# Optimization experiments

Hardware: AMD Instinct MI355X
Metric: run time of the kernel (lower is better)

The kernel has to match this reference:

```python
import jax, jax.numpy as jnp
import numpy as np

WH, WW = 16, 16
NUM_HEADS = 16
DIM = 1024
BATCH = 64
SEQ = WH * WW + 1  # 257, includes cls token
NUM_REL = (2 * WH - 1) * (2 * WW - 1) + 3  # 964


def _make_rel_pos_index(wh, ww):
    # BEiT relative position index construction (intended semantics of the torch code)
    coords = np.stack(np.meshgrid(np.arange(wh), np.arange(ww), indexing='ij'))  # [2, wh, ww]
    flat = coords.reshape(2, -1)  # [2, wh*ww]
    rel = flat[:, :, None] - flat[:, None, :]  # [2, N-1, N-1]
    rel = rel.transpose(1, 2, 0).astype(np.int64)
    rel[:, :, 0] += wh - 1
    rel[:, :, 1] += ww - 1
    rel[:, :, 0] *= 2 * ww - 1
    num_rel = (2 * wh - 1) * (2 * ww - 1) + 3
    idx = np.zeros((wh * ww + 1, wh * ww + 1), dtype=np.int32)
    idx[1:, 1:] = rel.sum(-1)
    idx[0, :] = num_rel - 3  # cls-to-token
    idx[:, 0] = num_rel - 2  # token-to-cls
    idx[0, 0] = num_rel - 1  # cls-to-cls
    return idx


def setup_inputs() -> dict:
    key = jax.random.key(0)
    ks = jax.random.split(key, 7)
    return {
        'x': jax.random.normal(ks[0], (BATCH, SEQ, DIM), dtype=jnp.float32),
        'qkv_weight': jax.random.normal(ks[1], (3 * DIM, DIM), dtype=jnp.float32) * 0.02,
        'query_bias': jax.random.normal(ks[2], (DIM,), dtype=jnp.float32) * 0.02,
        'value_bias': jax.random.normal(ks[3], (DIM,), dtype=jnp.float32) * 0.02,
        'rel_pos_bias_table': jax.random.normal(ks[4], (NUM_REL, NUM_HEADS), dtype=jnp.float32) * 0.02,
        'proj_weight': jax.random.normal(ks[5], (DIM, DIM), dtype=jnp.float32) * 0.02,
        'proj_bias': jax.random.normal(ks[6], (DIM,), dtype=jnp.float32) * 0.02,
        'rel_pos_index': jnp.asarray(_make_rel_pos_index(WH, WW)),
    }


def reference(x, qkv_weight, query_bias, value_bias, rel_pos_bias_table,
              proj_weight, proj_bias, rel_pos_index):
    B, N, C = x.shape
    H = rel_pos_bias_table.shape[-1]
    D = qkv_weight.shape[0] // 3 // H
    scale = D ** -0.5
    # qkv bias: (q_bias, zeros, v_bias) as in the torch module
    qkv_bias = jnp.concatenate([query_bias, jnp.zeros_like(value_bias), value_bias])
    qkv = x @ qkv_weight.T + qkv_bias  # [B, N, 3*H*D]
    qkv = qkv.reshape(B, N, 3, H, D).transpose(2, 0, 3, 1, 4)  # [3, B, H, N, D]
    q, k, v = qkv[0] * scale, qkv[1], qkv[2]
    attn = jnp.einsum('bhqd,bhkd->bhqk', q, k)  # [B, H, N, N]
    bias = rel_pos_bias_table[rel_pos_index]  # [N, N, H]
    attn = attn + bias.transpose(2, 0, 1)[None]  # add per-head bias
    attn = jax.nn.softmax(attn, axis=-1)
    out = jnp.einsum('bhqk,bhkd->bhqd', attn, v)  # [B, H, N, D]
    out = out.transpose(0, 2, 1, 3).reshape(B, N, H * D)
    return out @ proj_weight.T + proj_bias
```

## Files before the change

kernel.cpp:

```cpp
#include <hip/hip_runtime.h>


typedef unsigned short u16;
typedef __attribute__((ext_vector_type(8))) short bf16x8;
typedef __attribute__((ext_vector_type(4))) float f32x4;

#define MFMA16(a, b, c) __builtin_amdgcn_mfma_f32_16x16x32_bf16(a, b, c, 0, 0, 0)
#define GLDS16(g, l)                                                           \
  __builtin_amdgcn_global_load_lds(                                            \
      (const __attribute__((address_space(1))) void*)(g),                      \
      (__attribute__((address_space(3))) void*)(l), 16, 0, 0)

#define QOFF 0
#define KOFF 16842752
#define VTOFF 33685504
#define VTP 264

__device__ __forceinline__ u16 f2bf(float f) {
  unsigned u = __builtin_bit_cast(unsigned, f);
  u += 0x7FFFu + ((u >> 16) & 1u);
  return (u16)(u >> 16);
}
__device__ __forceinline__ unsigned pack2(float a, float b) {
  return (unsigned)f2bf(a) | ((unsigned)f2bf(b) << 16);
}

__global__ __launch_bounds__(256) void cvt_bf16(const float* __restrict__ in,
                                                u16* __restrict__ out, int n4) {
  int i = blockIdx.x * 256 + threadIdx.x;
  if (i < n4) {
    float4 v = ((const float4*)in)[i];
    uint2 o;
    o.x = pack2(v.x, v.y);
    o.y = pack2(v.z, v.w);
    ((uint2*)out)[i] = o;
  }
}

__global__ __launch_bounds__(256) void bias_pre(const float* __restrict__ tab,
                                                const int* __restrict__ idx,
                                                u16* __restrict__ out) {
  int t = blockIdx.x * 256 + threadIdx.x;
  if (t < 66049) {
    int i = t / 257, j = t - i * 257;
    int off = i * 288 + ((j >> 5) << 5) + ((j & 15) << 1) + ((j >> 4) & 1);
    int id = idx[t];
    const float* row = tab + (size_t)id * 16;
#pragma unroll
    for (int h = 0; h < 16; h++)
      out[(size_t)h * 74016 + off] = f2bf(row[h] * 1.4426950408889634f);
  } else if (t < 66049 + 257 * 31) {
    int u = t - 66049;
    int i = u / 31, j = 257 + (u - i * 31);
    int off = i * 288 + ((j >> 5) << 5) + ((j & 15) << 1) + ((j >> 4) & 1);
#pragma unroll
    for (int h = 0; h < 16; h++)
      out[(size_t)h * 74016 + off] = 0xFF7Fu;
  }
}


#define GEMM_PROLOG(M_, K_)                                                    \
  __shared__ __align__(16) u16 SMEM[16384];                                    \
  u16* const As = SMEM;                                                        \
  u16* const Bs = SMEM + 8192;                                                 \
  const int M = (M_), K = (K_);                                                \
  const int tid = threadIdx.x;                                                 \
  const int lane = tid & 63, wave = tid >> 6;                                  \
  const int quad = lane >> 4, l15 = lane & 15;                                 \
  const int wr = (wave >> 1) * 64, wc = (wave & 1) * 64;                       \
  const int m0 = blockIdx.y * 128, n0 = blockIdx.x * 128;                      \
  const int sgk = ((tid & 7) ^ ((tid >> 3) & 7)) * 8;    \
  const int fo0 = (quad ^ (l15 & 7)) * 8;            \
  const int fo1 = ((4 + quad) ^ (l15 & 7)) * 8;      \
  const u16* pa0 = A + (size_t)(m0 + (tid >> 3)) * K + sgk;                    \
  const u16* pb0 = B + (size_t)(n0 + (tid >> 3)) * K + sgk;                    \
  f32x4 acc[4][4];                                                             \
  _Pragma("unroll") for (int i = 0; i < 4; i++)                                \
  _Pragma("unroll") for (int j = 0; j < 4; j++)                                \
      acc[i][j] = (f32x4){0.f, 0.f, 0.f, 0.f};                                 \
  for (int k0 = 0; k0 < K; k0 += 64) {                                         \
    __syncthreads();                                                           \
    _Pragma("unroll") for (int b = 0; b < 4; b++) {                            \
      GLDS16(pa0 + k0 + (size_t)b * 32 * K, As + b * 2048 + tid * 8);          \
      GLDS16(pb0 + k0 + (size_t)b * 32 * K, Bs + b * 2048 + tid * 8);          \
    }                                                                          \
    __syncthreads();                                                           \
    _Pragma("unroll") for (int kk = 0; kk < 2; kk++) {                         \
      const int fo = kk ? fo1 : fo0;                                           \
      bf16x8 bfr[4];                                                           \
      _Pragma("unroll") for (int t = 0; t < 4; t++)                            \
          bfr[t] = *(const bf16x8*)(Bs + (wc + t * 16 + l15) * 64 + fo);       \
      _Pragma("unroll") for (int i = 0; i < 4; i++) {                          \
        bf16x8 afr = *(const bf16x8*)(As + (wr + i * 16 + l15) * 64 + fo);     \
        _Pragma("unroll") for (int j = 0; j < 4; j++)                          \
            acc[i][j] = MFMA16(afr, bfr[j], acc[i][j]);                        \
      }                                                                        \
    }                                                                          \
  }

__global__ __launch_bounds__(256, 4) void gemm_qkv(
    const u16* __restrict__ A, const u16* __restrict__ B,
    const float* __restrict__ qbias, const float* __restrict__ vbias,
    u16* __restrict__ C) {
  GEMM_PROLOG(16448, 1024)
  if (n0 >= 2048) {
    u16* const T = SMEM;
    for (int p = 0; p < 2; p++) {
      __syncthreads();
      if ((wave & 1) == p) {
#pragma unroll
        for (int j = 0; j < 4; j++) {
          int cl = j * 16 + l15;
          int rem = (n0 + wc + j * 16 + l15) & 1023;
          float vb_ = vbias[rem];
          int swz = (cl & 15) << 3;
#pragma unroll
          for (int i = 0; i < 4; i++) {
            int rlb = wr + i * 16 + quad * 4;
#pragma unroll
            for (int rr = 0; rr < 2; rr++) {
              unsigned pk = pack2(acc[i][j][rr * 2] + vb_,
                                  acc[i][j][rr * 2 + 1] + vb_);
              *(unsigned*)(T + cl * 128 + ((rlb + rr * 2) ^ swz)) = pk;
            }
          }
        }
      }
      __syncthreads();
#pragma unroll
      for (int cc = 0; cc < 16; cc++) {
        int cl = cc * 4 + wave;
        int rem = (n0 + p * 64 + cl) & 1023;
        int h = rem >> 6, d = rem & 63;
        size_t cb = (size_t)VTOFF + ((size_t)h * 64 + d) * VTP;
        int swz = (cl & 15) << 3;
#pragma unroll
        for (int half = 0; half < 2; half++) {
          int rl = half * 64 + lane;
          u16 val = T[cl * 128 + (rl ^ swz)];
          int m = m0 + rl;
          if (m < M) {
            unsigned bb2 = (unsigned)m / 257u;
            unsigned nn2 = (unsigned)m - bb2 * 257u;
            C[cb + (size_t)bb2 * (16 * 64 * VTP) + nn2] = val;
          }
        }
      }
    }
  } else {
#pragma unroll
    for (int i = 0; i < 4; i++) {
#pragma unroll
      for (int r = 0; r < 4; r++) {
        int row = m0 + wr + i * 16 + quad * 4 + r;
        if (row < M) {
          unsigned bb = (unsigned)row / 257u;
          unsigned nn = (unsigned)row - bb * 257u;
#pragma unroll
          for (int j = 0; j < 4; j++) {
            int c = n0 + wc + j * 16 + l15;
            int which = c >> 10, rem = c & 1023;
            float bias = (which == 0) ? qbias[rem] : 0.f;
            float v = acc[i][j][r] + bias;
            if (which == 0) v *= 0.18033688011112042f;
            int h = rem >> 6, d = rem & 63;
            size_t dst = (size_t)which * 16842752 +
                         (size_t)(bb * 16 + h) * 16448 + (size_t)nn * 64 + d;
            C[dst] = f2bf(v);
          }
        }
      }
    }
  }
}

__global__ __launch_bounds__(256, 4) void gemm_proj(
    const u16* __restrict__ A, const u16* __restrict__ B,
    const float* __restrict__ pbias, float* __restrict__ C) {
  GEMM_PROLOG(16448, 1024)
#pragma unroll
  for (int i = 0; i < 4; i++) {
#pragma unroll
    for (int r = 0; r < 4; r++) {
      int row = m0 + wr + i * 16 + quad * 4 + r;
      if (row < M) {
#pragma unroll
        for (int j = 0; j < 4; j++) {
          int c = n0 + wc + j * 16 + l15;
          C[(size_t)row * 1024 + c] = acc[i][j][r] + pbias[c];
        }
      }
    }
  }
}

__global__ __launch_bounds__(256, 3) void attn_fused(
    const u16* __restrict__ qkv, const u16* __restrict__ biasT,
    u16* __restrict__ out) {
  __shared__ __align__(16) u16 KVs[96 * 72];
  __shared__ __align__(16) u16 Ps[4 * 16 * 104];
  const int bx = blockIdx.x;
  const int xj = bx & 7, xi = bx >> 3;
  const int qt = xi % 5;
  const int bh = (xi / 5) * 8 + xj;
  const int b = bh >> 4, h = bh & 15;
  const int tid = threadIdx.x, lane = tid & 63, wave = tid >> 6;
  const int quad = lane >> 4, l15 = lane & 15;
  const bool act = (qt < 4) || (wave == 0);
  const u16* qg = qkv + QOFF + (size_t)bh * 16448;
  const u16* kg = qkv + KOFF + (size_t)bh * 16448;
  const u16* vtg = qkv + VTOFF + (size_t)bh * (64 * VTP);

  int qra = qt * 64 + wave * 16 + l15;
  if (qra > 256) qra = 256;
  const bf16x8 aq0 = *(const bf16x8*)(qg + (size_t)qra * 64 + quad * 8);
  const bf16x8 aq1 = *(const bf16x8*)(qg + (size_t)qra * 64 + 32 + quad * 8);

  const int qbase = qt * 64 + wave * 16 + quad * 4;
  f32x4 s[18];
  if (act) {
    const u16* bb = biasT + (size_t)h * 74016;
#pragma unroll
    for (int r = 0; r < 4; r++) {
      int qr = qbase + r;
      if (qr > 256) qr = 256;
      const unsigned* brow = (const unsigned*)(bb + (size_t)qr * 288);
#pragma unroll
      for (int p = 0; p < 9; p++) {
        unsigned u = brow[p * 16 + l15];
        s[2 * p][r] = __builtin_bit_cast(float, u << 16);
        s[2 * p + 1][r] = __builtin_bit_cast(float, u & 0xFFFF0000u);
      }
    }
  }

  const bf16x8 zv = {0, 0, 0, 0, 0, 0, 0, 0};
  for (int ck = 0; ck < 3; ck++) {
    __syncthreads();
#pragma unroll
    for (int it = 0; it < 3; it++) {
      int g = it * 256 + tid;
      int row = g >> 3, col = (g & 7) * 8;
      int gr = ck * 96 + row;
      bf16x8 kv = (gr < 257) ? *(const bf16x8*)(kg + (size_t)gr * 64 + col) : zv;
      *(bf16x8*)(KVs + row * 72 + col) = kv;
    }
    __syncthreads();
    if (act) {
#pragma unroll
      for (int nt = 0; nt < 6; nt++) {
        bf16x8 b0 = *(const bf16x8*)(KVs + (nt * 16 + l15) * 72 + quad * 8);
        bf16x8 b1 = *(const bf16x8*)(KVs + (nt * 16 + l15) * 72 + 32 + quad * 8);
        int t = ck * 6 + nt;
        s[t] = MFMA16(aq0, b0, s[t]);
        s[t] = MFMA16(aq1, b1, s[t]);
      }
    }
  }

  float inv[4];
  if (act) {
#pragma unroll
    for (int r = 0; r < 4; r++) {
      float m = -3e38f;
#pragma unroll
      for (int t = 0; t < 18; t++) m = fmaxf(m, s[t][r]);
      m = fmaxf(m, __shfl_xor(m, 1));
      m = fmaxf(m, __shfl_xor(m, 2));
      m = fmaxf(m, __shfl_xor(m, 4));
      m = fmaxf(m, __shfl_xor(m, 8));
      float sum = 0.f;
#pragma unroll
      for (int t = 0; t < 18; t++) {
        float p = __builtin_amdgcn_exp2f(s[t][r] - m);
        s[t][r] = p;
        sum += p;
      }
      sum += __shfl_xor(sum, 1);
      sum += __shfl_xor(sum, 2);
      sum += __shfl_xor(sum, 4);
      sum += __shfl_xor(sum, 8);
      inv[r] = 1.f / sum;
    }
  }

  u16* Pw = Ps + wave * (16 * 104);
  f32x4 o[4];
#pragma unroll
  for (int nt = 0; nt < 4; nt++) o[nt] = (f32x4){0.f, 0.f, 0.f, 0.f};
  for (int ck = 0; ck < 3; ck++) {
    __syncthreads();
#pragma unroll
    for (int it = 0; it < 3; it++) {
      int g = it * 256 + tid;
      int row = g / 12, c = (g % 12) * 8;
      bf16x8 v = *(const bf16x8*)(vtg + (size_t)row * VTP + ck * 96 + c);
      *(bf16x8*)(KVs + row * 104 + c) = v;
    }
    if (act) {
#pragma unroll
      for (int nt = 0; nt < 6; nt++) {
        int t = ck * 6 + nt;
#pragma unroll
        for (int r = 0; r < 4; r++)
          Pw[(quad * 4 + r) * 104 + nt * 16 + l15] = f2bf(s[t][r]);
      }
    }
    __syncthreads();
    if (act) {
#pragma unroll
      for (int ks = 0; ks < 3; ks++) {
        bf16x8 ap = *(const bf16x8*)(Pw + l15 * 104 + ks * 32 + quad * 8);
#pragma unroll
        for (int nt = 0; nt < 4; nt++) {
          bf16x8 bv =
              *(const bf16x8*)(KVs + (nt * 16 + l15) * 104 + ks * 32 + quad * 8);
          o[nt] = MFMA16(ap, bv, o[nt]);
        }
      }
    }
  }

  if (act) {
#pragma unroll
    for (int nt = 0; nt < 4; nt++) {
      int d = nt * 16 + l15;
#pragma unroll
      for (int r = 0; r < 4; r++) {
        int qr = qbase + r;
        if (qr < 257)
          out[((size_t)b * 257 + qr) * 1024 + h * 64 + d] =
              f2bf(o[nt][r] * inv[r]);
      }
    }
  }
}

extern "C" void kernel_launch(void* const* d_in, const int* in_sizes, int n_in,
                              void* d_out, int out_size, void* d_ws,
                              size_t ws_size, hipStream_t stream) {
  const float* x = (const float*)d_in[0];
  const float* qkvw = (const float*)d_in[1];
  const float* qb = (const float*)d_in[2];
  const float* vb = (const float*)d_in[3];
  const float* tab = (const float*)d_in[4];
  const float* pw = (const float*)d_in[5];
  const float* pb = (const float*)d_in[6];
  const int* rpi = (const int*)d_in[7];

  char* ws = (char*)d_ws;
  u16* qkvbuf = (u16*)ws;
  u16* xbuf = (u16*)(ws + 101974016);
  u16* biasb = (u16*)(ws + 135659520);
  u16* qkvwb = (u16*)(ws + 139886656);
  u16* projwb = (u16*)(ws + 146178112);

  cvt_bf16<<<16448, 256, 0, stream>>>(x, xbuf, 4210688);
  cvt_bf16<<<3072, 256, 0, stream>>>(qkvw, qkvwb, 786432);
  cvt_bf16<<<1024, 256, 0, stream>>>(pw, projwb, 262144);
  bias_pre<<<290, 256, 0, stream>>>(tab, rpi, biasb);
  gemm_qkv<<<dim3(24, 129), 256, 0, stream>>>(xbuf, qkvwb, qb, vb, qkvbuf);
  attn_fused<<<5120, 256, 0, stream>>>(qkvbuf, biasb, xbuf);
  gemm_proj<<<dim3(8, 129), 256, 0, stream>>>(xbuf, projwb, pb, (float*)d_out);
}
```

Baseline: 418.7 us.

## Double-buffer GEMM K-loop with 32-wide tiles to overlap loads and MFMA

Restructures the shared GEMM mainloop from a single-buffered 64-wide K tile into a ping-pong double buffer of 32-wide K tiles. The next tile's global-to-LDS load is issued before computing the current one, so there is one barrier per step instead of two. The XOR swizzle is adjusted for the narrower rows. It hardcodes K=1024 (32 tiles), which ties the macro to that K, and it halves the MFMA work available between barriers.

```diff
diff --git a/kernel.cpp b/kernel.cpp
--- a/kernel.cpp
+++ b/kernel.cpp
@@ -60,44 +60,58 @@
 }
 
 
+#define GSTAGE(BO, TI)                                                         \
+  GLDS16(pa0 + (TI) * 32, SMEM + (BO) + tid * 8);                              \
+  GLDS16(pa1 + (TI) * 32, SMEM + (BO) + 2048 + tid * 8);                       \
+  GLDS16(pb0 + (TI) * 32, SMEM + (BO) + 4096 + tid * 8);                       \
+  GLDS16(pb1 + (TI) * 32, SMEM + (BO) + 6144 + tid * 8);
+
+#define GCOMPUTE(BO)                                                           \
+  {                                                                            \
+    const u16* As_ = SMEM + (BO);                                              \
+    const u16* Bs_ = SMEM + (BO) + 4096;                                       \
+    bf16x8 bfr[4];                                                             \
+    _Pragma("unroll") for (int t = 0; t < 4; t++)                              \
+        bfr[t] = *(const bf16x8*)(Bs_ + (wc + t * 16 + l15) * 32 + fo);        \
+    _Pragma("unroll") for (int i = 0; i < 4; i++) {                            \
+      bf16x8 afr = *(const bf16x8*)(As_ + (wr + i * 16 + l15) * 32 + fo);      \
+      _Pragma("unroll") for (int j = 0; j < 4; j++)                            \
+          acc[i][j] = MFMA16(afr, bfr[j], acc[i][j]);                          \
+    }                                                                          \
+  }
+
 #define GEMM_PROLOG(M_, K_)                                                    \
   __shared__ __align__(16) u16 SMEM[16384];                                    \
-  u16* const As = SMEM;                                                        \
-  u16* const Bs = SMEM + 8192;                                                 \
   const int M = (M_), K = (K_);                                                \
   const int tid = threadIdx.x;                                                 \
   const int lane = tid & 63, wave = tid >> 6;                                  \
   const int quad = lane >> 4, l15 = lane & 15;                                 \
   const int wr = (wave >> 1) * 64, wc = (wave & 1) * 64;                       \
   const int m0 = blockIdx.y * 128, n0 = blockIdx.x * 128;                      \
-  const int sgk = ((tid & 7) ^ ((tid >> 3) & 7)) * 8;    \
-  const int fo0 = (quad ^ (l15 & 7)) * 8;            \
-  const int fo1 = ((4 + quad) ^ (l15 & 7)) * 8;      \
-  const u16* pa0 = A + (size_t)(m0 + (tid >> 3)) * K + sgk;                    \
-  const u16* pb0 = B + (size_t)(n0 + (tid >> 3)) * K + sgk;                    \
+  const int sgk = (((tid & 3) ^ ((tid >> 3) & 3))) * 8;  \
+  const int fo = ((quad ^ ((l15 >> 1) & 3))) * 8;         \
+  const u16* pa0 = A + (size_t)(m0 + (tid >> 2)) * K + sgk;                    \
+  const u16* pa1 = pa0 + (size_t)64 * K;                                       \
+  const u16* pb0 = B + (size_t)(n0 + (tid >> 2)) * K + sgk;                    \
+  const u16* pb1 = pb0 + (size_t)64 * K;                                       \
   f32x4 acc[4][4];                                                             \
   _Pragma("unroll") for (int i = 0; i < 4; i++)                                \
   _Pragma("unroll") for (int j = 0; j < 4; j++)                                \
       acc[i][j] = (f32x4){0.f, 0.f, 0.f, 0.f};                                 \
-  for (int k0 = 0; k0 < K; k0 += 64) {                                         \
+  GSTAGE(0, 0)                                                                 \
+  __syncthreads();                                                             \
+  for (int kt = 0; kt < 30; kt += 2) {                                         \
+    GSTAGE(8192, kt + 1)                                                       \
+    GCOMPUTE(0)                                                                \
     __syncthreads();                                                           \
-    _Pragma("unroll") for (int b = 0; b < 4; b++) {                            \
-      GLDS16(pa0 + k0 + (size_t)b * 32 * K, As + b * 2048 + tid * 8);          \
-      GLDS16(pb0 + k0 + (size_t)b * 32 * K, Bs + b * 2048 + tid * 8);          \
-    }                                                                          \
+    GSTAGE(0, kt + 2)                                                          \
+    GCOMPUTE(8192)                                                             \
     __syncthreads();                                                           \
-    _Pragma("unroll") for (int kk = 0; kk < 2; kk++) {                         \
-      const int fo = kk ? fo1 : fo0;                                           \
-      bf16x8 bfr[4];                                                           \
-      _Pragma("unroll") for (int t = 0; t < 4; t++)                            \
-          bfr[t] = *(const bf16x8*)(Bs + (wc + t * 16 + l15) * 64 + fo);       \
-      _Pragma("unroll") for (int i = 0; i < 4; i++) {                          \
-        bf16x8 afr = *(const bf16x8*)(As + (wr + i * 16 + l15) * 64 + fo);     \
-        _Pragma("unroll") for (int j = 0; j < 4; j++)                          \
-            acc[i][j] = MFMA16(afr, bfr[j], acc[i][j]);                        \
-      }                                                                        \
-    }                                                                          \
-  }
+  }                                                                            \
+  GSTAGE(8192, 31)                                                             \
+  GCOMPUTE(0)                                                                  \
+  __syncthreads();                                                             \
+  GCOMPUTE(8192)
 
 __global__ __launch_bounds__(256, 4) void gemm_qkv(
     const u16* __restrict__ A, const u16* __restrict__ B,
```

After: 407.2 us. 1.03x faster.
